# Performance work log

Hardware: AMD Instinct MI355X
Metric: run time of the kernel (lower is better)

The kernel has to match this reference:

```python
import jax, jax.numpy as jnp
import numpy as np

B_, L, DM = 2, 1024, 1024
D_STATE, D_CONV, EXPAND = 16, 4, 2
DI = EXPAND * DM          # 2048 inner dim
DTR = DM // 16            # 64 dt rank


def setup_inputs() -> dict:
    key = jax.random.key(0)
    ks = jax.random.split(key, 16)
    g = lambda k, shp, s: jax.random.normal(k, shp, jnp.float32) * s
    inp = {
        "x": g(ks[0], (B_, L, DM), 1.0),
        "ln_g": jnp.ones((DM,), jnp.float32),
        "ln_b": jnp.zeros((DM,), jnp.float32),
        "in_proj_w": g(ks[1], (2 * DI, DM), (2.0 / (DM + 2 * DI)) ** 0.5),
        "conv_w": g(ks[2], (DI, 1, D_CONV), (2.0 / D_CONV) ** 0.5),
        "conv_b": jnp.zeros((DI,), jnp.float32),
        "dtin_w": g(ks[3], (DTR, DI), (2.0 / (DI + DTR)) ** 0.5),
        "dtin_b": jnp.zeros((DTR,), jnp.float32),
        "dt_w": g(ks[4], (DI, DTR), DTR ** -0.5),
        "dt_b": jnp.log(jnp.expm1(jax.random.uniform(ks[5], (DI,), jnp.float32, 1e-3, 0.1))),  # inverse-softplus of dt in [dt_min, dt_max]
        "B_w": g(ks[6], (D_STATE, DI), DI ** -0.5),
        "C_w": g(ks[7], (D_STATE, DI), DI ** -0.5),
        "A_log": jnp.log(jnp.broadcast_to(jnp.arange(1, D_STATE + 1, dtype=jnp.float32), (DI, D_STATE))),
        "D": jnp.ones((DI,), jnp.float32),
        "out_w": g(ks[8], (DM, DI), (2.0 / (DM + DI)) ** 0.5),
    }
    return inp


def _layernorm(x, g, b, eps=1e-5):
    mu = jnp.mean(x, -1, keepdims=True)
    var = jnp.mean(jnp.square(x - mu), -1, keepdims=True)
    return (x - mu) * jax.lax.rsqrt(var + eps) * g + b


def _selective_scan(u, dt, Bm, Cm, A, Dp):
    # u,dt: (b,l,di); Bm,Cm: (b,l,n); A: (di,n)
    def step(h, inp):
        dt_t, B_t, C_t, u_t = inp  # (b,di),(b,n),(b,n),(b,di)
        dA = jnp.exp(dt_t[..., None] * A)                       # (b,di,n)
        h = h * dA + (dt_t * u_t)[..., None] * B_t[:, None, :]   # (b,di,n)
        y = jnp.einsum("bdn,bn->bd", h, C_t)
        return h, y

    tm = lambda a: jnp.swapaxes(a, 0, 1)  # time-major
    h0 = jnp.zeros((u.shape[0], u.shape[2], A.shape[1]), u.dtype)
    _, ys = jax.lax.scan(step, h0, (tm(dt), tm(Bm), tm(Cm), tm(u)))
    return jnp.swapaxes(ys, 0, 1) + u * Dp  # (b,l,di)


def reference(x, ln_g, ln_b, in_proj_w, conv_w, conv_b, dtin_w, dtin_b,
              dt_w, dt_b, B_w, C_w, A_log, D, out_w):
    residual = x
    xn = _layernorm(x, ln_g, ln_b)
    xz = xn @ in_proj_w.T                       # (b,l,2*di)
    x_proj, z = jnp.split(xz, 2, axis=-1)
    # causal depthwise conv1d (left pad d_conv-1, truncate to seq_len)
    xp = jnp.pad(x_proj, ((0, 0), (D_CONV - 1, 0), (0, 0)))
    x_conv = conv_b
    for k in range(D_CONV):
        x_conv = x_conv + conv_w[:, 0, k] * xp[:, k:k + L, :]
    x_conv = jax.nn.silu(x_conv)
    dt_in = x_conv @ dtin_w.T + dtin_b          # (b,l,dtr)
    dt = jax.nn.softplus(dt_in @ dt_w.T + dt_b) # (b,l,di)
    Bm = x_conv @ B_w.T                         # (b,l,n)
    Cm = x_conv @ C_w.T
    A = -jnp.exp(A_log)                         # (di,n)
    y = _selective_scan(x_conv, dt, Bm, Cm, A, D)
    y = y * jax.nn.silu(z)
    return y @ out_w.T + residual
```

## Files before the change

kernel.cpp:

```cpp
#include <hip/hip_runtime.h>
#include <hip/hip_bf16.h>
#include <cstdint>

#define BL    2
#define LSEQ  1024
#define DMOD  1024
#define DIN   2048
#define NST   16
#define DTRK  64
#define MR    (BL*LSEQ)

#define CCH 32
#define TCH 32
#define KSPLIT 8

typedef __bf16 bf16x8 __attribute__((ext_vector_type(8)));
typedef float  f32x4  __attribute__((ext_vector_type(4)));

#if __has_builtin(__builtin_amdgcn_exp2f)
#define EXP2F(x) __builtin_amdgcn_exp2f(x)
#else
#define EXP2F(x) exp2f(x)
#endif
#define LOG2E 1.4426950408889634f

__device__ __forceinline__ void glds16(const void* g, const void* l) {
    __builtin_amdgcn_global_load_lds(
        (__attribute__((address_space(1))) void*)(uintptr_t)(g),
        (__attribute__((address_space(3))) void*)(uint32_t)(uintptr_t)(l),
        16, 0, 0);
}

template <int MODE, int TM, int TN, int BK>
__global__ __launch_bounds__(256, 3) void gemm_bt(
    const __hip_bfloat16* __restrict__ A, int lda,
    const __hip_bfloat16* __restrict__ Bw, int ldb,
    int M, int N, int Ksl,
    void* __restrict__ e0, void* __restrict__ e1,
    const float* __restrict__ bias, const float* __restrict__ bias2)
{
    constexpr bool FUSE = (MODE == 0);
    static_assert(!FUSE || BK == 64, "fused conv epilogue assumes BK=64");
    constexpr int WM = TM / 2, WN = TN / 2;
    constexpr int MT = WM / 16, NT = WN / 16;
    constexpr int C8 = BK / 8;
    constexpr int RPP = 256 / C8;
    constexpr int PA = TM / RPP, PB = TN / RPP;
    __shared__ __align__(16) __hip_bfloat16 sA[2][TM * BK];
    __shared__ __align__(16) __hip_bfloat16 sB[2][TN * BK];
    __shared__ __align__(16) __hip_bfloat16 sH[2][(FUSE ? 16 : 1) * 64];

    auto SW = [](int row) { return (BK == 32) ? ((row >> 1) & 3) : (row & 7); };

    int bx = blockIdx.x, by = blockIdx.y;
    if ((gridDim.y & 7) == 0) {
        const int bid = blockIdx.x + gridDim.x * blockIdx.y;
        const int xcd = bid & 7, s = bid >> 3;
        bx = s % gridDim.x;
        by = (s / gridDim.x) * 8 + xcd;
    }
    const int m0 = by * TM;
    const int n0 = bx * TN;
    const int k0 = blockIdx.z * Ksl;
    const int tid = threadIdx.x;
    const int w = tid >> 6, lane = tid & 63;
    const int wm = (w >> 1) * WM, wn = (w & 1) * WN;
    const int lrow = lane & 15, lq = lane >> 4;

    const int r0 = tid / C8;
    const int q = ((tid % C8) - SW(r0)) & (C8 - 1);
    const __hip_bfloat16* pa[PA];
    const __hip_bfloat16* pb[PB];
#pragma unroll
    for (int p = 0; p < PA; p++) pa[p] = A + (size_t)(m0 + r0 + RPP * p) * lda + k0 + q * 8;
#pragma unroll
    for (int p = 0; p < PB; p++) pb[p] = Bw + (size_t)(n0 + r0 + RPP * p) * ldb + k0 + q * 8;

    const bool isX = FUSE && (n0 < DIN);
    const __hip_bfloat16* ph = nullptr;
    if (FUSE) {
        const int rh = tid >> 3;
        const int qh = ((tid & 7) - (rh & 7)) & 7;
        ph = A + (size_t)(m0 - 16 + rh) * lda + k0 + qh * 8;
    }

    f32x4 acc[MT][NT];
#pragma unroll
    for (int i = 0; i < MT; i++)
#pragma unroll
        for (int j = 0; j < NT; j++) { acc[i][j][0]=0.f; acc[i][j][1]=0.f; acc[i][j][2]=0.f; acc[i][j][3]=0.f; }
    f32x4 hacc[FUSE ? NT : 1];
    if (FUSE)
#pragma unroll
        for (int j = 0; j < NT; j++) { hacc[j][0]=0.f; hacc[j][1]=0.f; hacc[j][2]=0.f; hacc[j][3]=0.f; }

    const int nk = Ksl / BK;
#pragma unroll
    for (int p = 0; p < PA; p++) glds16(pa[p], &sA[0][(tid + 256 * p) * 8]);
#pragma unroll
    for (int p = 0; p < PB; p++) glds16(pb[p], &sB[0][(tid + 256 * p) * 8]);
    if (isX && tid < 128) glds16(ph, &sH[0][tid * 8]);

    for (int kb = 0; kb < nk; ++kb) {
        const int cur = kb & 1, nxt = cur ^ 1;
        __syncthreads();
        if (kb + 1 < nk) {
#pragma unroll
            for (int p = 0; p < PA; p++) { pa[p] += BK; glds16(pa[p], &sA[nxt][(tid + 256 * p) * 8]); }
#pragma unroll
            for (int p = 0; p < PB; p++) { pb[p] += BK; glds16(pb[p], &sB[nxt][(tid + 256 * p) * 8]); }
            if (isX && tid < 128) { ph += BK; glds16(ph, &sH[nxt][tid * 8]); }
        }
#pragma unroll
        for (int s = 0; s < BK / 32; s++) {
            bf16x8 af[MT], bb[NT];
#pragma unroll
            for (int mt = 0; mt < MT; mt++) {
                const int row = wm + mt * 16 + lrow;
                const int pc = ((s * 4 + lq) + SW(row)) & (C8 - 1);
                af[mt] = *(const bf16x8*)&sA[cur][row * BK + pc * 8];
            }
#pragma unroll
            for (int nt = 0; nt < NT; nt++) {
                const int row = wn + nt * 16 + lrow;
                const int pc = ((s * 4 + lq) + SW(row)) & (C8 - 1);
                bb[nt] = *(const bf16x8*)&sB[cur][row * BK + pc * 8];
            }
#pragma unroll
            for (int mt = 0; mt < MT; mt++)
#pragma unroll
                for (int nt = 0; nt < NT; nt++)
                    acc[mt][nt] = __builtin_amdgcn_mfma_f32_16x16x32_bf16(af[mt], bb[nt], acc[mt][nt], 0, 0, 0);
            if (isX && w < 2) {
                const int pcH = ((s * 4 + lq) + (lrow & 7)) & 7;
                const bf16x8 afh = *(const bf16x8*)&sH[cur][lrow * 64 + pcH * 8];
#pragma unroll
                for (int nt = 0; nt < NT; nt++)
                    hacc[nt] = __builtin_amdgcn_mfma_f32_16x16x32_bf16(afh, bb[nt], hacc[nt], 0, 0, 0);
            }
        }
    }

    if (MODE == 0 && isX) {
        __syncthreads();
        __hip_bfloat16* tile = (__hip_bfloat16*)&sB[0][0];
        constexpr int TS = TN + 8;
#pragma unroll
        for (int mt = 0; mt < MT; mt++)
#pragma unroll
            for (int nt = 0; nt < NT; nt++) {
                const int col = wn + nt * 16 + lrow;
#pragma unroll
                for (int r = 0; r < 4; r++)
                    tile[(16 + wm + mt * 16 + lq * 4 + r) * TS + col] = __float2bfloat16(acc[mt][nt][r]);
            }
        if (w < 2) {
#pragma unroll
            for (int nt = 0; nt < NT; nt++) {
                const int col = wn + nt * 16 + lrow;
#pragma unroll
                for (int r = 0; r < 4; r++)
                    tile[(lq * 4 + r) * TS + col] = __float2bfloat16(hacc[nt][r]);
            }
        }
        __syncthreads();
        const int c2 = (tid & 63) * 2;
        const int rg = tid >> 6;
        const int dg = n0 + c2;
        const float4 wA = *(const float4*)&bias[dg * 4];
        const float4 wB = *(const float4*)&bias[dg * 4 + 4];
        const float cbA = bias2[dg], cbB = bias2[dg + 1];
        const int l0 = m0 & (LSEQ - 1);
        const int rbase = rg * 16;
        float a0, a1, a2, b0, b1, b2;
        if (l0 == 0 && rg == 0) {
            a0 = a1 = a2 = b0 = b1 = b2 = 0.f;
        } else {
            const int hr = 16 + rbase - 3;
            a0 = __bfloat162float(tile[(hr + 0) * TS + c2]);
            b0 = __bfloat162float(tile[(hr + 0) * TS + c2 + 1]);
            a1 = __bfloat162float(tile[(hr + 1) * TS + c2]);
            b1 = __bfloat162float(tile[(hr + 1) * TS + c2 + 1]);
            a2 = __bfloat162float(tile[(hr + 2) * TS + c2]);
            b2 = __bfloat162float(tile[(hr + 2) * TS + c2 + 1]);
        }
        __hip_bfloat16* xcbp = (__hip_bfloat16*)e0;
#pragma unroll 4
        for (int i = 0; i < 16; i++) {
            const int row = rbase + i;
            const float a3 = __bfloat162float(tile[(16 + row) * TS + c2]);
            const float b3 = __bfloat162float(tile[(16 + row) * TS + c2 + 1]);
            float sa = cbA + wA.x * a0 + wA.y * a1 + wA.z * a2 + wA.w * a3;
            float sb = cbB + wB.x * b0 + wB.y * b1 + wB.z * b2 + wB.w * b3;
            sa = sa / (1.f + __expf(-sa));
            sb = sb / (1.f + __expf(-sb));
            __hip_bfloat16 ha = __float2bfloat16(sa), hb = __float2bfloat16(sb);
            ushort2 o;
            o.x = (unsigned short)__hip_bfloat16_raw(ha).x;
            o.y = (unsigned short)__hip_bfloat16_raw(hb).x;
            *(ushort2*)&xcbp[(size_t)(m0 + row) * DIN + dg] = o;
            a0 = a1; a1 = a2; a2 = a3;
            b0 = b1; b1 = b2; b2 = b3;
        }
        return;
    }
#pragma unroll
    for (int mt = 0; mt < MT; mt++) {
#pragma unroll
        for (int nt = 0; nt < NT; nt++) {
            const int gn = n0 + wn + nt * 16 + lrow;
            if (gn >= N) continue;
            const int gmb = m0 + wm + mt * 16 + lq * 4;
#pragma unroll
            for (int r = 0; r < 4; r++) {
                const int gm = gmb + r;
                const float v = acc[mt][nt][r];
                if (MODE == 0) {
                    const float s = v / (1.f + __expf(-v));
                    ((__hip_bfloat16*)e1)[(size_t)gm * DIN + (gn - DIN)] = __float2bfloat16(s);
                } else if (MODE == 1) {
                    ((float*)e0)[((size_t)blockIdx.z * M + gm) * 96 + gn] = v;
                } else if (MODE == 2) {
                    const float xx = v + bias[gn];
                    const float sp = (xx > 20.f) ? xx : log1pf(__expf(xx));
                    ((__hip_bfloat16*)e0)[(size_t)gm * N + gn] = __float2bfloat16(sp);
                } else {
                    ((float*)e0)[(size_t)gm * N + gn] = v + ((const float*)e1)[(size_t)gm * N + gn];
                }
            }
        }
    }
}

__global__ void ep1_kernel(const float* __restrict__ part, const float* __restrict__ dtin_b,
                           __hip_bfloat16* __restrict__ dtinb, float* __restrict__ Bmf,
                           float* __restrict__ Cmf) {
    const int i = blockIdx.x * 256 + threadIdx.x;
    if (i >= MR * 96) return;
    const int m = i / 96, n = i - m * 96;
    float s = 0.f;
#pragma unroll
    for (int z = 0; z < KSPLIT; z++) s += part[((size_t)z * MR + m) * 96 + n];
    if (n < 64)      dtinb[(size_t)m * 64 + n] = __float2bfloat16(s + dtin_b[n]);
    else if (n < 80) Bmf[(size_t)m * NST + (n - 64)] = s;
    else             Cmf[(size_t)m * NST + (n - 80)] = s;
}

#define NCVT 1654784
__global__ void prep_kernel(const float* __restrict__ x, const float* __restrict__ ln_g,
                            const float* __restrict__ ln_b,
                            const float* __restrict__ w_in, const float* __restrict__ dtin_w,
                            const float* __restrict__ B_w, const float* __restrict__ C_w,
                            const float* __restrict__ dt_w, const float* __restrict__ out_w,
                            __hip_bfloat16* __restrict__ w1b, __hip_bfloat16* __restrict__ wpb,
                            __hip_bfloat16* __restrict__ dtwb, __hip_bfloat16* __restrict__ owb,
                            __hip_bfloat16* __restrict__ xn)
{
    const int b = blockIdx.x;
    const int tid = threadIdx.x;
    if (b < MR) {
        const float4 v = ((const float4*)(x + (size_t)b * DMOD))[tid];
        float s  = v.x + v.y + v.z + v.w;
        float sq = v.x * v.x + v.y * v.y + v.z * v.z + v.w * v.w;
#pragma unroll
        for (int off = 32; off >= 1; off >>= 1) {
            s  += __shfl_down(s, off, 64);
            sq += __shfl_down(sq, off, 64);
        }
        __shared__ float red[8];
        const int w = tid >> 6, lane = tid & 63;
        if (lane == 0) { red[w] = s; red[4 + w] = sq; }
        __syncthreads();
        s  = red[0] + red[1] + red[2] + red[3];
        sq = red[4] + red[5] + red[6] + red[7];
        const float mean = s * (1.f / DMOD);
        const float rstd = rsqrtf(sq * (1.f / DMOD) - mean * mean + 1e-5f);
        const int col = tid * 4;
        const float vv[4] = {v.x, v.y, v.z, v.w};
#pragma unroll
        for (int i = 0; i < 4; i++)
            xn[(size_t)b * DMOD + col + i] =
                __float2bfloat16((vv[i] - mean) * rstd * ln_g[col + i] + ln_b[col + i]);
        return;
    }
    const int nb = gridDim.x - MR;
    for (int v4 = (b - MR) * 256 + tid; v4 < NCVT; v4 += nb * 256) {
        const int i = v4 * 4;
        const float* s; __hip_bfloat16* dk;
        if      (i < 4194304) { s = w_in   + i;             dk = w1b  + i; }
        else if (i < 4325376) { s = dtin_w + (i - 4194304); dk = wpb  + (i - 4194304); }
        else if (i < 4358144) { s = B_w    + (i - 4325376); dk = wpb  + 131072 + (i - 4325376); }
        else if (i < 4390912) { s = C_w    + (i - 4358144); dk = wpb  + 163840 + (i - 4358144); }
        else if (i < 4521984) { s = dt_w   + (i - 4390912); dk = dtwb + (i - 4390912); }
        else                  { s = out_w  + (i - 4521984); dk = owb  + (i - 4521984); }
        const float4 f = *(const float4*)s;
        ushort4 o;
        o.x = (unsigned short)(__hip_bfloat16_raw(__float2bfloat16(f.x)).x);
        o.y = (unsigned short)(__hip_bfloat16_raw(__float2bfloat16(f.y)).x);
        o.z = (unsigned short)(__hip_bfloat16_raw(__float2bfloat16(f.z)).x);
        o.w = (unsigned short)(__hip_bfloat16_raw(__float2bfloat16(f.w)).x);
        *(ushort4*)dk = o;
    }
}


__global__ __launch_bounds__(256) void scan_p1(
    const __hip_bfloat16* __restrict__ dt, const __hip_bfloat16* __restrict__ u,
    const float* __restrict__ Bm, const float* __restrict__ A_log,
    float* __restrict__ Aprod, float* __restrict__ Bacc)
{
    __shared__ float sB[TCH * NST];
    const int blk = blockIdx.x;
    const int bb = blk >> 9, c = (blk >> 4) & 31, dtile = blk & 15;
    const int tid = threadIdx.x;
    const int nh = tid & 1, dl = tid >> 1;
    const int d = dtile * 128 + dl;
    const int row0 = bb * LSEQ + c * TCH;

    sB[tid]       = Bm[(size_t)row0 * NST + tid];
    sB[tid + 256] = Bm[(size_t)row0 * NST + tid + 256];
    __syncthreads();

    float a2[8];
    {
        const float4 al0 = *(const float4*)&A_log[(size_t)d * NST + nh * 8];
        const float4 al1 = *(const float4*)&A_log[(size_t)d * NST + nh * 8 + 4];
        a2[0] = -__expf(al0.x) * LOG2E; a2[1] = -__expf(al0.y) * LOG2E;
        a2[2] = -__expf(al0.z) * LOG2E; a2[3] = -__expf(al0.w) * LOG2E;
        a2[4] = -__expf(al1.x) * LOG2E; a2[5] = -__expf(al1.y) * LOG2E;
        a2[6] = -__expf(al1.z) * LOG2E; a2[7] = -__expf(al1.w) * LOG2E;
    }
    const __hip_bfloat16* pdt = dt + (size_t)row0 * DIN + d;
    const __hip_bfloat16* pu  = u  + (size_t)row0 * DIN + d;
    float h[8], Ap[8];
#pragma unroll
    for (int j = 0; j < 8; j++) { h[j] = 0.f; Ap[j] = 1.f; }

#pragma unroll 4
    for (int t = 0; t < TCH; t++) {
        const float dtv = __bfloat162float(pdt[t * DIN]);
        const float uv  = __bfloat162float(pu[t * DIN]);
        const float du = dtv * uv;
        float bv[8];
        *(float4*)&bv[0] = *(const float4*)&sB[t * NST + nh * 8];
        *(float4*)&bv[4] = *(const float4*)&sB[t * NST + nh * 8 + 4];
#pragma unroll
        for (int j = 0; j < 8; j++) {
            const float e = EXP2F(dtv * a2[j]);
            Ap[j] *= e;
            h[j] = h[j] * e + du * bv[j];
        }
    }
    const size_t idx = (((size_t)bb * CCH + c) * DIN + d) * NST + nh * 8;
    *(float4*)&Aprod[idx]     = make_float4(Ap[0], Ap[1], Ap[2], Ap[3]);
    *(float4*)&Aprod[idx + 4] = make_float4(Ap[4], Ap[5], Ap[6], Ap[7]);
    *(float4*)&Bacc[idx]      = make_float4(h[0], h[1], h[2], h[3]);
    *(float4*)&Bacc[idx + 4]  = make_float4(h[4], h[5], h[6], h[7]);
}

__global__ __launch_bounds__(256) void scan_p2(
    const float* __restrict__ Aprod, const float* __restrict__ Bacc,
    float* __restrict__ hstart)
{
    const int i = blockIdx.x * 256 + threadIdx.x;
    const int bb = i >> 15;
    const int dn = i & 32767;
    float hs = 0.f;
#pragma unroll
    for (int c = 0; c < CCH; c++) {
        const size_t idx = (((size_t)bb * CCH + c) << 15) + dn;
        hstart[idx] = hs;
        hs = Aprod[idx] * hs + Bacc[idx];
    }
}

__global__ __launch_bounds__(256) void scan_p3(
    const __hip_bfloat16* __restrict__ dt, const __hip_bfloat16* __restrict__ u,
    const float* __restrict__ Bm, const float* __restrict__ Cm,
    const float* __restrict__ A_log, const float* __restrict__ Dp,
    const __hip_bfloat16* __restrict__ zs, const float* __restrict__ hstart,
    __hip_bfloat16* __restrict__ y)
{
    __shared__ float sB[TCH * NST], sC[TCH * NST];
    const int blk = blockIdx.x;
    const int bb = blk >> 9, c = (blk >> 4) & 31, dtile = blk & 15;
    const int tid = threadIdx.x;
    const int nh = tid & 1, dl = tid >> 1;
    const int d = dtile * 128 + dl;
    const int row0 = bb * LSEQ + c * TCH;

    sB[tid]       = Bm[(size_t)row0 * NST + tid];
    sB[tid + 256] = Bm[(size_t)row0 * NST + tid + 256];
    sC[tid]       = Cm[(size_t)row0 * NST + tid];
    sC[tid + 256] = Cm[(size_t)row0 * NST + tid + 256];
    __syncthreads();

    float a2[8];
    {
        const float4 al0 = *(const float4*)&A_log[(size_t)d * NST + nh * 8];
        const float4 al1 = *(const float4*)&A_log[(size_t)d * NST + nh * 8 + 4];
        a2[0] = -__expf(al0.x) * LOG2E; a2[1] = -__expf(al0.y) * LOG2E;
        a2[2] = -__expf(al0.z) * LOG2E; a2[3] = -__expf(al0.w) * LOG2E;
        a2[4] = -__expf(al1.x) * LOG2E; a2[5] = -__expf(al1.y) * LOG2E;
        a2[6] = -__expf(al1.z) * LOG2E; a2[7] = -__expf(al1.w) * LOG2E;
    }
    const float Dd = Dp[d];
    const size_t idx = (((size_t)bb * CCH + c) * DIN + d) * NST + nh * 8;
    float h[8];
    *(float4*)&h[0] = *(const float4*)&hstart[idx];
    *(float4*)&h[4] = *(const float4*)&hstart[idx + 4];

    const __hip_bfloat16* pdt = dt + (size_t)row0 * DIN + d;
    const __hip_bfloat16* pu  = u  + (size_t)row0 * DIN + d;
    const __hip_bfloat16* pz  = zs + (size_t)row0 * DIN + d;
    __hip_bfloat16* py = y + (size_t)row0 * DIN + d;

#pragma unroll 2
    for (int t = 0; t < TCH; t++) {
        const float dtv = __bfloat162float(pdt[t * DIN]);
        const float uv  = __bfloat162float(pu[t * DIN]);
        const float du = dtv * uv;
        float bv[8], cv[8];
        *(float4*)&bv[0] = *(const float4*)&sB[t * NST + nh * 8];
        *(float4*)&bv[4] = *(const float4*)&sB[t * NST + nh * 8 + 4];
        *(float4*)&cv[0] = *(const float4*)&sC[t * NST + nh * 8];
        *(float4*)&cv[4] = *(const float4*)&sC[t * NST + nh * 8 + 4];
        float yp = 0.f;
#pragma unroll
        for (int j = 0; j < 8; j++) {
            const float e = EXP2F(dtv * a2[j]);
            h[j] = h[j] * e + du * bv[j];
            yp += h[j] * cv[j];
        }
        yp += __shfl_xor(yp, 1, 64);
        if (nh == 0) {
            const float zv = __bfloat162float(pz[t * DIN]);
            py[t * DIN] = __float2bfloat16((yp + uv * Dd) * zv);
        }
    }
}

extern "C" void kernel_launch(void* const* d_in, const int* in_sizes, int n_in,
                              void* d_out, int out_size, void* d_ws, size_t ws_size,
                              hipStream_t stream) {
    const float* x      = (const float*)d_in[0];
    const float* ln_g   = (const float*)d_in[1];
    const float* ln_b   = (const float*)d_in[2];
    const float* w_in   = (const float*)d_in[3];
    const float* conv_w = (const float*)d_in[4];
    const float* conv_b = (const float*)d_in[5];
    const float* dtin_w = (const float*)d_in[6];
    const float* dtin_b = (const float*)d_in[7];
    const float* dt_w   = (const float*)d_in[8];
    const float* dt_b   = (const float*)d_in[9];
    const float* B_w    = (const float*)d_in[10];
    const float* C_w    = (const float*)d_in[11];
    const float* A_log  = (const float*)d_in[12];
    const float* Dp     = (const float*)d_in[13];
    const float* out_w  = (const float*)d_in[14];
    float* out = (float*)d_out;

    char* ws = (char*)d_ws;
    auto alloc = [&](size_t bytes) { char* p = ws; ws += (bytes + 255) & ~255ull; return p; };
    __hip_bfloat16* w1b   = (__hip_bfloat16*)alloc((size_t)4096 * 1024 * 2);
    __hip_bfloat16* wpb   = (__hip_bfloat16*)alloc((size_t)96 * 2048 * 2);
    __hip_bfloat16* dtwb  = (__hip_bfloat16*)alloc((size_t)2048 * 64 * 2);
    __hip_bfloat16* owb   = (__hip_bfloat16*)alloc((size_t)1024 * 2048 * 2);
    __hip_bfloat16* xnb   = (__hip_bfloat16*)alloc((size_t)MR * DMOD * 2);
    __hip_bfloat16* zs    = (__hip_bfloat16*)alloc((size_t)MR * DIN * 2);
    __hip_bfloat16* xcb   = (__hip_bfloat16*)alloc((size_t)MR * DIN * 2);
    __hip_bfloat16* dtinb = (__hip_bfloat16*)alloc((size_t)MR * 64 * 2);
    float*          Bmf   = (float*)alloc((size_t)MR * NST * 4);
    float*          Cmf   = (float*)alloc((size_t)MR * NST * 4);
    __hip_bfloat16* dtb   = (__hip_bfloat16*)alloc((size_t)MR * DIN * 2);
    __hip_bfloat16* yb    = (__hip_bfloat16*)alloc((size_t)MR * DIN * 2);
    float*          Aprod = (float*)alloc((size_t)BL * CCH * DIN * NST * 4);
    float*          Bacc  = (float*)alloc((size_t)BL * CCH * DIN * NST * 4);
    float*          hstart= (float*)alloc((size_t)BL * CCH * DIN * NST * 4);
    float*          part  = (float*)w1b;

    prep_kernel<<<MR + 896, 256, 0, stream>>>(x, ln_g, ln_b, w_in, dtin_w, B_w, C_w, dt_w,
                                              out_w, w1b, wpb, dtwb, owb, xnb);

    gemm_bt<0, 64, 128, 64><<<dim3(32, 32, 1), 256, 0, stream>>>(
        xnb, 1024, w1b, 1024, MR, 4096, 1024, xcb, zs, conv_w, conv_b);

    gemm_bt<1, 64, 128, 64><<<dim3(1, 32, KSPLIT), 256, 0, stream>>>(
        xcb, 2048, wpb, 2048, MR, 96, 2048 / KSPLIT, part, nullptr, nullptr, nullptr);
    ep1_kernel<<<(MR * 96 + 255) / 256, 256, 0, stream>>>(part, dtin_b, dtinb, Bmf, Cmf);

    gemm_bt<2, 64, 128, 64><<<dim3(16, 32, 1), 256, 0, stream>>>(
        dtinb, 64, dtwb, 64, MR, DIN, 64, dtb, nullptr, dt_b, nullptr);

    scan_p1<<<BL * CCH * 16, 256, 0, stream>>>(dtb, xcb, Bmf, A_log, Aprod, Bacc);
    scan_p2<<<BL * DIN * NST / 256, 256, 0, stream>>>(Aprod, Bacc, hstart);
    scan_p3<<<BL * CCH * 16, 256, 0, stream>>>(dtb, xcb, Bmf, Cmf, A_log, Dp, zs, hstart, yb);

    gemm_bt<3, 64, 64, 64><<<dim3(16, 32, 1), 256, 0, stream>>>(
        yb, 2048, owb, 2048, MR, DMOD, 2048, out, (void*)x, nullptr, nullptr);
}
```

Measured before the change: 233.5 us.

## Fuse dt projection into scan kernels and reduce split-K via atomics

Removes the separate dt GEMM and split-K reduction kernel. The split-K partials for dt_in, B and C are now accumulated with float atomics into a buffer zeroed in the prep kernel. The dtin bias is folded through dt_w into a per-channel offset precomputed in prep. Each scan_p1/scan_p3 block recomputes its 32x128 dt tile with MFMA in shared memory, avoiding the full dt write and re-read. In exchange the dt tile is computed twice, the kernels use more LDS, and atomics make summation order nondeterministic.

```diff
diff --git a/kernel.cpp b/kernel.cpp
--- a/kernel.cpp
+++ b/kernel.cpp
@@ -29,6 +29,11 @@
         (__attribute__((address_space(1))) void*)(uintptr_t)(g),
         (__attribute__((address_space(3))) void*)(uint32_t)(uintptr_t)(l),
         16, 0, 0);
+}
+
+__device__ __forceinline__ __bf16 f2b(float f) {
+    __hip_bfloat16 t = __float2bfloat16(f);
+    return *(__bf16*)&t;
 }
 
 template <int MODE, int TM, int TN, int BK>
@@ -219,11 +224,9 @@
                     const float s = v / (1.f + __expf(-v));
                     ((__hip_bfloat16*)e1)[(size_t)gm * DIN + (gn - DIN)] = __float2bfloat16(s);
                 } else if (MODE == 1) {
-                    ((float*)e0)[((size_t)blockIdx.z * M + gm) * 96 + gn] = v;
-                } else if (MODE == 2) {
-                    const float xx = v + bias[gn];
-                    const float sp = (xx > 20.f) ? xx : log1pf(__expf(xx));
-                    ((__hip_bfloat16*)e0)[(size_t)gm * N + gn] = __float2bfloat16(sp);
+                    if (gn < 64)      atomicAdd((float*)e0 + (size_t)gm * 64 + gn, v);
+                    else if (gn < 80) atomicAdd((float*)e1 + (size_t)gm * NST + (gn - 64), v);
+                    else              atomicAdd((float*)e1 + (size_t)MR * NST + (size_t)gm * NST + (gn - 80), v);
                 } else {
                     ((float*)e0)[(size_t)gm * N + gn] = v + ((const float*)e1)[(size_t)gm * N + gn];
                 }
@@ -232,29 +235,19 @@
     }
 }
 
-__global__ void ep1_kernel(const float* __restrict__ part, const float* __restrict__ dtin_b,
-                           __hip_bfloat16* __restrict__ dtinb, float* __restrict__ Bmf,
-                           float* __restrict__ Cmf) {
-    const int i = blockIdx.x * 256 + threadIdx.x;
-    if (i >= MR * 96) return;
-    const int m = i / 96, n = i - m * 96;
-    float s = 0.f;
-#pragma unroll
-    for (int z = 0; z < KSPLIT; z++) s += part[((size_t)z * MR + m) * 96 + n];
-    if (n < 64)      dtinb[(size_t)m * 64 + n] = __float2bfloat16(s + dtin_b[n]);
-    else if (n < 80) Bmf[(size_t)m * NST + (n - 64)] = s;
-    else             Cmf[(size_t)m * NST + (n - 80)] = s;
-}
-
 #define NCVT 1654784
+#define NZR  49152
+#define NOFF 2048
 __global__ void prep_kernel(const float* __restrict__ x, const float* __restrict__ ln_g,
                             const float* __restrict__ ln_b,
                             const float* __restrict__ w_in, const float* __restrict__ dtin_w,
                             const float* __restrict__ B_w, const float* __restrict__ C_w,
                             const float* __restrict__ dt_w, const float* __restrict__ out_w,
+                            const float* __restrict__ dtin_b, const float* __restrict__ dt_b,
                             __hip_bfloat16* __restrict__ w1b, __hip_bfloat16* __restrict__ wpb,
                             __hip_bfloat16* __restrict__ dtwb, __hip_bfloat16* __restrict__ owb,
-                            __hip_bfloat16* __restrict__ xn)
+                            __hip_bfloat16* __restrict__ xn, float* __restrict__ zblock,
+                            float* __restrict__ off)
 {
     const int b = blockIdx.x;
     const int tid = threadIdx.x;
@@ -263,9 +256,9 @@
         float s  = v.x + v.y + v.z + v.w;
         float sq = v.x * v.x + v.y * v.y + v.z * v.z + v.w * v.w;
 #pragma unroll
-        for (int off = 32; off >= 1; off >>= 1) {
-            s  += __shfl_down(s, off, 64);
-            sq += __shfl_down(sq, off, 64);
+        for (int off_ = 32; off_ >= 1; off_ >>= 1) {
+            s  += __shfl_down(s, off_, 64);
+            sq += __shfl_down(sq, off_, 64);
         }
         __shared__ float red[8];
         const int w = tid >> 6, lane = tid & 63;
@@ -284,42 +277,128 @@
         return;
     }
     const int nb = gridDim.x - MR;
-    for (int v4 = (b - MR) * 256 + tid; v4 < NCVT; v4 += nb * 256) {
-        const int i = v4 * 4;
-        const float* s; __hip_bfloat16* dk;
-        if      (i < 4194304) { s = w_in   + i;             dk = w1b  + i; }
-        else if (i < 4325376) { s = dtin_w + (i - 4194304); dk = wpb  + (i - 4194304); }
-        else if (i < 4358144) { s = B_w    + (i - 4325376); dk = wpb  + 131072 + (i - 4325376); }
-        else if (i < 4390912) { s = C_w    + (i - 4358144); dk = wpb  + 163840 + (i - 4358144); }
-        else if (i < 4521984) { s = dt_w   + (i - 4390912); dk = dtwb + (i - 4390912); }
-        else                  { s = out_w  + (i - 4521984); dk = owb  + (i - 4521984); }
-        const float4 f = *(const float4*)s;
-        ushort4 o;
-        o.x = (unsigned short)(__hip_bfloat16_raw(__float2bfloat16(f.x)).x);
-        o.y = (unsigned short)(__hip_bfloat16_raw(__float2bfloat16(f.y)).x);
-        o.z = (unsigned short)(__hip_bfloat16_raw(__float2bfloat16(f.z)).x);
-        o.w = (unsigned short)(__hip_bfloat16_raw(__float2bfloat16(f.w)).x);
-        *(ushort4*)dk = o;
-    }
-}
-
+    for (int v4 = (b - MR) * 256 + tid; v4 < NCVT + NZR + NOFF; v4 += nb * 256) {
+        if (v4 < NCVT) {
+            const int i = v4 * 4;
+            const float* s; __hip_bfloat16* dk;
+            if      (i < 4194304) { s = w_in   + i;             dk = w1b  + i; }
+            else if (i < 4325376) { s = dtin_w + (i - 4194304); dk = wpb  + (i - 4194304); }
+            else if (i < 4358144) { s = B_w    + (i - 4325376); dk = wpb  + 131072 + (i - 4325376); }
+            else if (i < 4390912) { s = C_w    + (i - 4358144); dk = wpb  + 163840 + (i - 4358144); }
+            else if (i < 4521984) { s = dt_w   + (i - 4390912); dk = dtwb + (i - 4390912); }
+            else                  { s = out_w  + (i - 4521984); dk = owb  + (i - 4521984); }
+            const float4 f = *(const float4*)s;
+            ushort4 o;
+            o.x = (unsigned short)(__hip_bfloat16_raw(__float2bfloat16(f.x)).x);
+            o.y = (unsigned short)(__hip_bfloat16_raw(__float2bfloat16(f.y)).x);
+            o.z = (unsigned short)(__hip_bfloat16_raw(__float2bfloat16(f.z)).x);
+            o.w = (unsigned short)(__hip_bfloat16_raw(__float2bfloat16(f.w)).x);
+            *(ushort4*)dk = o;
+        } else if (v4 < NCVT + NZR) {
+            float4 z; z.x = z.y = z.z = z.w = 0.f;
+            ((float4*)zblock)[v4 - NCVT] = z;
+        } else {
+            const int d = v4 - NCVT - NZR;
+            const float4* wr = (const float4*)(dt_w + (size_t)d * 64);
+            const float4* br = (const float4*)dtin_b;
+            float s = dt_b[d];
+#pragma unroll
+            for (int i = 0; i < 16; i++) {
+                const float4 a = wr[i], c = br[i];
+                s += a.x * c.x + a.y * c.y + a.z * c.z + a.w * c.w;
+            }
+            off[d] = s;
+        }
+    }
+}
+
+
+__device__ __forceinline__ void compute_dt_tile(
+    const float* __restrict__ fdtin, const __hip_bfloat16* __restrict__ dtw,
+    const float* __restrict__ off, int row0, int d0, int tid,
+    __hip_bfloat16* sDI, __hip_bfloat16* sDW, __hip_bfloat16* sDT)
+{
+    const int lane = tid & 63, lrow = lane & 15, lq = lane >> 4, wv = tid >> 6;
+    {
+        const int rr = tid >> 3, cq = tid & 7;
+        const float* src = fdtin + (size_t)(row0 + rr) * 64 + cq * 8;
+        const float4 f0 = *(const float4*)src;
+        const float4 f1 = *(const float4*)(src + 4);
+        bf16x8 o;
+        o[0] = f2b(f0.x); o[1] = f2b(f0.y); o[2] = f2b(f0.z); o[3] = f2b(f0.w);
+        o[4] = f2b(f1.x); o[5] = f2b(f1.y); o[6] = f2b(f1.z); o[7] = f2b(f1.w);
+        *(bf16x8*)&sDI[rr * 64 + (((cq) + (rr & 7)) & 7) * 8] = o;
+    }
+#pragma unroll
+    for (int p = 0; p < 4; p++) {
+        const int rr = p * 32 + (tid >> 3);
+        const int q = ((tid & 7) - (rr & 7)) & 7;
+        glds16(dtw + (size_t)(d0 + rr) * 64 + q * 8, &sDW[(p * 256 + tid) * 8]);
+    }
+    __syncthreads();
+    f32x4 dacc[2][2];
+#pragma unroll
+    for (int i = 0; i < 2; i++)
+#pragma unroll
+        for (int j = 0; j < 2; j++) { dacc[i][j][0]=0.f; dacc[i][j][1]=0.f; dacc[i][j][2]=0.f; dacc[i][j][3]=0.f; }
+#pragma unroll
+    for (int s = 0; s < 2; s++) {
+        bf16x8 af[2], bf_[2];
+#pragma unroll
+        for (int mt = 0; mt < 2; mt++) {
+            const int rr = mt * 16 + lrow;
+            af[mt] = *(const bf16x8*)&sDI[rr * 64 + (((s * 4 + lq) + (rr & 7)) & 7) * 8];
+        }
+#pragma unroll
+        for (int ntl = 0; ntl < 2; ntl++) {
+            const int rr = wv * 32 + ntl * 16 + lrow;
+            bf_[ntl] = *(const bf16x8*)&sDW[rr * 64 + (((s * 4 + lq) + (rr & 7)) & 7) * 8];
+        }
+#pragma unroll
+        for (int mt = 0; mt < 2; mt++)
+#pragma unroll
+            for (int ntl = 0; ntl < 2; ntl++)
+                dacc[mt][ntl] = __builtin_amdgcn_mfma_f32_16x16x32_bf16(af[mt], bf_[ntl], dacc[mt][ntl], 0, 0, 0);
+    }
+#pragma unroll
+    for (int mt = 0; mt < 2; mt++)
+#pragma unroll
+        for (int ntl = 0; ntl < 2; ntl++) {
+            const int dcol = wv * 32 + ntl * 16 + lrow;
+            const float offv = off[d0 + dcol];
+#pragma unroll
+            for (int r = 0; r < 4; r++) {
+                const int t = mt * 16 + lq * 4 + r;
+                const float xx = dacc[mt][ntl][r] + offv;
+                const float sp = (xx > 20.f) ? xx : log1pf(__expf(xx));
+                sDT[t * 128 + dcol] = __float2bfloat16(sp);
+            }
+        }
+    __syncthreads();
+}
 
 __global__ __launch_bounds__(256) void scan_p1(
-    const __hip_bfloat16* __restrict__ dt, const __hip_bfloat16* __restrict__ u,
-    const float* __restrict__ Bm, const float* __restrict__ A_log,
+    const float* __restrict__ fdtin, const __hip_bfloat16* __restrict__ dtw,
+    const float* __restrict__ off,
+    const __hip_bfloat16* __restrict__ u, const float* __restrict__ Bm,
+    const float* __restrict__ A_log,
     float* __restrict__ Aprod, float* __restrict__ Bacc)
 {
     __shared__ float sB[TCH * NST];
+    __shared__ __align__(16) __hip_bfloat16 sDI[32 * 64];
+    __shared__ __align__(16) __hip_bfloat16 sDW[128 * 64];
+    __shared__ __hip_bfloat16 sDT[32 * 128];
     const int blk = blockIdx.x;
     const int bb = blk >> 9, c = (blk >> 4) & 31, dtile = blk & 15;
     const int tid = threadIdx.x;
     const int nh = tid & 1, dl = tid >> 1;
-    const int d = dtile * 128 + dl;
+    const int d0 = dtile * 128;
+    const int d = d0 + dl;
     const int row0 = bb * LSEQ + c * TCH;
 
     sB[tid]       = Bm[(size_t)row0 * NST + tid];
     sB[tid + 256] = Bm[(size_t)row0 * NST + tid + 256];
-    __syncthreads();
+    compute_dt_tile(fdtin, dtw, off, row0, d0, tid, sDI, sDW, sDT);
 
     float a2[8];
     {
@@ -330,15 +409,14 @@
         a2[4] = -__expf(al1.x) * LOG2E; a2[5] = -__expf(al1.y) * LOG2E;
         a2[6] = -__expf(al1.z) * LOG2E; a2[7] = -__expf(al1.w) * LOG2E;
     }
-    const __hip_bfloat16* pdt = dt + (size_t)row0 * DIN + d;
-    const __hip_bfloat16* pu  = u  + (size_t)row0 * DIN + d;
+    const __hip_bfloat16* pu = u + (size_t)row0 * DIN + d;
     float h[8], Ap[8];
 #pragma unroll
     for (int j = 0; j < 8; j++) { h[j] = 0.f; Ap[j] = 1.f; }
 
 #pragma unroll 4
     for (int t = 0; t < TCH; t++) {
-        const float dtv = __bfloat162float(pdt[t * DIN]);
+        const float dtv = __bfloat162float(sDT[t * 128 + dl]);
         const float uv  = __bfloat162float(pu[t * DIN]);
         const float du = dtv * uv;
         float bv[8];
@@ -375,25 +453,30 @@
 }
 
 __global__ __launch_bounds__(256) void scan_p3(
-    const __hip_bfloat16* __restrict__ dt, const __hip_bfloat16* __restrict__ u,
-    const float* __restrict__ Bm, const float* __restrict__ Cm,
-    const float* __restrict__ A_log, const float* __restrict__ Dp,
-    const __hip_bfloat16* __restrict__ zs, const float* __restrict__ hstart,
-    __hip_bfloat16* __restrict__ y)
+    const float* __restrict__ fdtin, const __hip_bfloat16* __restrict__ dtw,
+    const float* __restrict__ off,
+    const __hip_bfloat16* __restrict__ u, const float* __restrict__ Bm,
+    const float* __restrict__ Cm, const float* __restrict__ A_log,
+    const float* __restrict__ Dp, const __hip_bfloat16* __restrict__ zs,
+    const float* __restrict__ hstart, __hip_bfloat16* __restrict__ y)
 {
     __shared__ float sB[TCH * NST], sC[TCH * NST];
+    __shared__ __align__(16) __hip_bfloat16 sDI[32 * 64];
+    __shared__ __align__(16) __hip_bfloat16 sDW[128 * 64];
+    __shared__ __hip_bfloat16 sDT[32 * 128];
     const int blk = blockIdx.x;
     const int bb = blk >> 9, c = (blk >> 4) & 31, dtile = blk & 15;
     const int tid = threadIdx.x;
     const int nh = tid & 1, dl = tid >> 1;
-    const int d = dtile * 128 + dl;
+    const int d0 = dtile * 128;
+    const int d = d0 + dl;
     const int row0 = bb * LSEQ + c * TCH;
 
     sB[tid]       = Bm[(size_t)row0 * NST + tid];
     sB[tid + 256] = Bm[(size_t)row0 * NST + tid + 256];
     sC[tid]       = Cm[(size_t)row0 * NST + tid];
     sC[tid + 256] = Cm[(size_t)row0 * NST + tid + 256];
-    __syncthreads();
+    compute_dt_tile(fdtin, dtw, off, row0, d0, tid, sDI, sDW, sDT);
 
     float a2[8];
     {
@@ -410,14 +493,13 @@
     *(float4*)&h[0] = *(const float4*)&hstart[idx];
     *(float4*)&h[4] = *(const float4*)&hstart[idx + 4];
 
-    const __hip_bfloat16* pdt = dt + (size_t)row0 * DIN + d;
-    const __hip_bfloat16* pu  = u  + (size_t)row0 * DIN + d;
-    const __hip_bfloat16* pz  = zs + (size_t)row0 * DIN + d;
+    const __hip_bfloat16* pu = u  + (size_t)row0 * DIN + d;
+    const __hip_bfloat16* pz = zs + (size_t)row0 * DIN + d;
     __hip_bfloat16* py = y + (size_t)row0 * DIN + d;
 
 #pragma unroll 2
     for (int t = 0; t < TCH; t++) {
-        const float dtv = __bfloat162float(pdt[t * DIN]);
+        const float dtv = __bfloat162float(sDT[t * 128 + dl]);
         const float uv  = __bfloat162float(pu[t * DIN]);
         const float du = dtv * uv;
         float bv[8], cv[8];
@@ -469,32 +551,30 @@
     __hip_bfloat16* xnb   = (__hip_bfloat16*)alloc((size_t)MR * DMOD * 2);
     __hip_bfloat16* zs    = (__hip_bfloat16*)alloc((size_t)MR * DIN * 2);
     __hip_bfloat16* xcb   = (__hip_bfloat16*)alloc((size_t)MR * DIN * 2);
-    __hip_bfloat16* dtinb = (__hip_bfloat16*)alloc((size_t)MR * 64 * 2);
-    float*          Bmf   = (float*)alloc((size_t)MR * NST * 4);
-    float*          Cmf   = (float*)alloc((size_t)MR * NST * 4);
-    __hip_bfloat16* dtb   = (__hip_bfloat16*)alloc((size_t)MR * DIN * 2);
     __hip_bfloat16* yb    = (__hip_bfloat16*)alloc((size_t)MR * DIN * 2);
+    float*          zblock= (float*)alloc((size_t)196608 * 4);
+    float*          off   = (float*)alloc((size_t)2048 * 4);
     float*          Aprod = (float*)alloc((size_t)BL * CCH * DIN * NST * 4);
     float*          Bacc  = (float*)alloc((size_t)BL * CCH * DIN * NST * 4);
     float*          hstart= (float*)alloc((size_t)BL * CCH * DIN * NST * 4);
-    float*          part  = (float*)w1b;
+
+    float* fdtin = zblock;
+    float* Bmf   = zblock + 131072;
 
     prep_kernel<<<MR + 896, 256, 0, stream>>>(x, ln_g, ln_b, w_in, dtin_w, B_w, C_w, dt_w,
-                                              out_w, w1b, wpb, dtwb, owb, xnb);
+                                              out_w, dtin_b, dt_b, w1b, wpb, dtwb, owb,
+                                              xnb, zblock, off);
 
     gemm_bt<0, 64, 128, 64><<<dim3(32, 32, 1), 256, 0, stream>>>(
         xnb, 1024, w1b, 1024, MR, 4096, 1024, xcb, zs, conv_w, conv_b);
 
     gemm_bt<1, 64, 128, 64><<<dim3(1, 32, KSPLIT), 256, 0, stream>>>(
-        xcb, 2048, wpb, 2048, MR, 96, 2048 / KSPLIT, part, nullptr, nullptr, nullptr);
-    ep1_kernel<<<(MR * 96 + 255) / 256, 256, 0, stream>>>(part, dtin_b, dtinb, Bmf, Cmf);
-
-    gemm_bt<2, 64, 128, 64><<<dim3(16, 32, 1), 256, 0, stream>>>(
-        dtinb, 64, dtwb, 64, MR, DIN, 64, dtb, nullptr, dt_b, nullptr);
-
-    scan_p1<<<BL * CCH * 16, 256, 0, stream>>>(dtb, xcb, Bmf, A_log, Aprod, Bacc);
+        xcb, 2048, wpb, 2048, MR, 96, 2048 / KSPLIT, fdtin, Bmf, nullptr, nullptr);
+
+    scan_p1<<<BL * CCH * 16, 256, 0, stream>>>(fdtin, dtwb, off, xcb, Bmf, A_log, Aprod, Bacc);
     scan_p2<<<BL * DIN * NST / 256, 256, 0, stream>>>(Aprod, Bacc, hstart);
-    scan_p3<<<BL * CCH * 16, 256, 0, stream>>>(dtb, xcb, Bmf, Cmf, A_log, Dp, zs, hstart, yb);
+    scan_p3<<<BL * CCH * 16, 256, 0, stream>>>(fdtin, dtwb, off, xcb, Bmf, Bmf + (size_t)MR * NST,
+                                               A_log, Dp, zs, hstart, yb);
 
     gemm_bt<3, 64, 64, 64><<<dim3(16, 32, 1), 256, 0, stream>>>(
         yb, 2048, owb, 2048, MR, DMOD, 2048, out, (void*)x, nullptr, nullptr);
```

Measured after the change: 243.7 us. 4.3% more time.
